# Kernel optimization log

Measured on AMD Instinct MI355X. Metric: run time of the kernel, lower is better.

## Reference

```python
import jax, jax.numpy as jnp
import numpy as np

BN_EPS = 1e-5
L1_EPS = 1e-12


def setup_inputs() -> dict:
    key = jax.random.key(0)
    k1, k2, k3, k4 = jax.random.split(key, 4)
    B, N, M, F = 16, 2048, 12, 64
    bond = 128
    atom = jax.random.normal(k1, (B, N, F), dtype=jnp.float32)
    adj = jax.random.randint(k2, (B, N * M, 2), 0, N, dtype=jnp.int64)
    stdv = 1.0 / np.sqrt(bond)
    W = jax.random.uniform(k3, (2 * F, bond), dtype=jnp.float32, minval=-stdv, maxval=stdv)
    b = jax.random.uniform(k4, (bond,), dtype=jnp.float32, minval=-stdv, maxval=stdv)
    gamma = jnp.ones((bond,), dtype=jnp.float32)
    beta = jnp.zeros((bond,), dtype=jnp.float32)
    return {"atom": atom, "adj": adj, "W": W, "b": b, "gamma": gamma, "beta": beta}


def reference(atom, adj, W, b, gamma, beta):
    B, N, F = atom.shape
    # flatten the (E,2) index pairs and gather atom features: (B, 2E, F)
    idx = adj.reshape(B, -1)
    gathered = jnp.take_along_axis(atom, idx[:, :, None], axis=1)
    # pair features per edge: (B, E, 2F)
    x = gathered.reshape(B, -1, 2 * F)
    # L1 normalize along the edge dim (dim=-2), matching F.normalize(p=1, dim=-2)
    denom = jnp.maximum(jnp.sum(jnp.abs(x), axis=1, keepdims=True), L1_EPS)
    x = x / denom
    # linear: (B, E, bond)
    x = jnp.einsum('bef,fc->bec', x, W) + b
    # BatchNorm1d (training mode): stats over batch and edge dims per channel
    mean = jnp.mean(x, axis=(0, 1))
    var = jnp.mean(jnp.square(x - mean), axis=(0, 1))  # biased variance
    x = (x - mean) * jax.lax.rsqrt(var + BN_EPS) * gamma + beta
    return jnp.tanh(x)
```

## Files before the change

kernel.cpp:

```cpp
#include <hip/hip_runtime.h>

#define B 16
#define N 2048
#define F 64
#define E 24576
#define C 128

typedef unsigned int uint32;
typedef unsigned short ushort16;
typedef float fvec4 __attribute__((ext_vector_type(4)));
typedef int   ivec2 __attribute__((ext_vector_type(2)));


__device__ __forceinline__ ushort16 f2bf(float f) {
    uint32 u = __float_as_uint(f);
    u += 0x7fffu + ((u >> 16) & 1u);
    return (ushort16)(u >> 16);
}
__device__ __forceinline__ float bf_lo(uint32 v) { return __uint_as_float(v << 16); }
__device__ __forceinline__ float bf_hi(uint32 v) { return __uint_as_float(v & 0xffff0000u); }

__global__ __launch_bounds__(256) void k_count(const int* __restrict__ adj,
                                               int* __restrict__ cnt) {
    int i = blockIdx.x * 256 + threadIdx.x;
    int n = adj[i];
    int k = i & 1;
    int b = i / (E * 2);
    atomicAdd(&cnt[(b * N + n) * 2 + k], 1);
}

__global__ __launch_bounds__(256) void k_denom(const float* __restrict__ atom,
                                               const int* __restrict__ cnt,
                                               float* __restrict__ denom) {
    int bid = blockIdx.x;
    int b = bid & 15;
    int chunk = bid >> 4;
    int t = threadIdx.x;
    int ch = t & 127;
    int sub = t >> 7;
    int half = ch >> 6;
    int f = ch & 63;
    float s = 0.f;
    int n0 = chunk * 128 + sub * 64;
    for (int j = 0; j < 64; ++j) {
        int n = n0 + j;
        float cf = (float)cnt[(b * N + n) * 2 + half];
        s = fmaf(cf, fabsf(atom[(b * N + n) * 64 + f]), s);
    }
    __shared__ float sd[256];
    sd[t] = s;
    __syncthreads();
    if (t < 128) atomicAdd(&denom[b * C + ch], sd[t] + sd[t + 128]);
}

__global__ __launch_bounds__(256, 2) void k_p(const float* __restrict__ atom,
                                              const float* __restrict__ W,
                                              const float* __restrict__ denom,
                                              const int* __restrict__ cnt,
                                              ushort16* __restrict__ P,
                                              float* __restrict__ nodew,
                                              float* __restrict__ nodesq) {
    int bid = blockIdx.x;
    int b = bid & 15;
    int chunk = bid >> 4;
    int t = threadIdx.x;
    int cp = t & 127;
    int half = cp >> 6;
    int c = cp & 63;
    int sub = t >> 7;

    __shared__ float invd[128];
    __shared__ float A2[64 * 128];
    __shared__ float cnts[2][64];

    if (t < 128) invd[t] = 1.0f / fmaxf(denom[b * C + t], 1e-12f);
    int nbase = chunk * 64;
    if (t < 128) {
        int h = t >> 6, r = t & 63;
        cnts[h][r] = (float)cnt[(b * N + nbase + r) * 2 + h];
    }
    __syncthreads();

    for (int i = t; i < 64 * 128; i += 256) {
        int r = i >> 7, col = i & 127;
        float a = atom[(b * N + nbase + r) * 64 + (col & 63)];
        A2[i] = a * invd[col];
    }

    float wreg0[64], wreg1[64];
#pragma unroll
    for (int f = 0; f < 64; ++f) {
        wreg0[f] = W[(half * 64 + f) * 128 + c];
        wreg1[f] = W[(half * 64 + f) * 128 + c + 64];
    }

    __syncthreads();

    float s1a = 0.f, s2a = 0.f, s1b = 0.f, s2b = 0.f;
    int r0 = sub * 32;
    for (int r = r0; r < r0 + 32; ++r) {
        const float* a = &A2[r * 128 + half * 64];
        float acc0 = 0.f, acc1 = 0.f;
#pragma unroll
        for (int f = 0; f < 64; f += 4) {
            float4 av = *(const float4*)(a + f);
            acc0 = fmaf(av.x, wreg0[f], acc0);
            acc0 = fmaf(av.y, wreg0[f + 1], acc0);
            acc0 = fmaf(av.z, wreg0[f + 2], acc0);
            acc0 = fmaf(av.w, wreg0[f + 3], acc0);
            acc1 = fmaf(av.x, wreg1[f], acc1);
            acc1 = fmaf(av.y, wreg1[f + 1], acc1);
            acc1 = fmaf(av.z, wreg1[f + 2], acc1);
            acc1 = fmaf(av.w, wreg1[f + 3], acc1);
        }
        float cw = cnts[half][r];
        s1a = fmaf(cw, acc0, s1a);
        s2a = fmaf(cw * acc0, acc0, s2a);
        s1b = fmaf(cw, acc1, s1b);
        s2b = fmaf(cw * acc1, acc1, s2b);
        size_t base = ((size_t)(b * N + nbase + r)) * 256 + half * 128;
        P[base + c]      = f2bf(acc0);
        P[base + c + 64] = f2bf(acc1);
    }
    atomicAdd(&nodew[b * 256 + half * 128 + c],      s1a);
    atomicAdd(&nodew[b * 256 + half * 128 + c + 64], s1b);
    atomicAdd(&nodesq[b * 128 + c],      s2a);
    atomicAdd(&nodesq[b * 128 + c + 64], s2b);
}

__global__ __launch_bounds__(256) void k_out(const ivec2* __restrict__ adj2,
                                             const uint2* __restrict__ Pu2,
                                             const float* __restrict__ nodew,
                                             const float* __restrict__ nodesq,
                                             const float* __restrict__ gamma,
                                             const float* __restrict__ beta,
                                             fvec4* __restrict__ out4) {
    int bid = blockIdx.x;
    int b = bid & 15;
    int chunk = bid >> 4;
    int t = threadIdx.x;
    __shared__ float ssc[128], ssh[128];
    __shared__ ivec2 eadj[512];

    int e0 = chunk * 512;
    const ivec2* ab = &adj2[(size_t)b * E + e0];
    eadj[t]       = __builtin_nontemporal_load(&ab[t]);
    eadj[t + 256] = __builtin_nontemporal_load(&ab[t + 256]);

    if (t < 128) {
        int cch = t;
        float m = 0.f, q = 0.f;
        const float invE = 1.0f / (float)E;
#pragma unroll
        for (int b2 = 0; b2 < B; ++b2) {
            float S0 = nodew[b2 * 256 + cch];
            float S1 = nodew[b2 * 256 + 128 + cch];
            m += S0 + S1;
            q += nodesq[b2 * 128 + cch] + 2.0f * S0 * S1 * invE;
        }
        const float inv = 1.0f / (float)(B * E);
        float mean_d = m * inv;
        float var = fmaxf(q * inv - mean_d * mean_d, 0.f);
        float sc = gamma[cch] * rsqrtf(var + 1e-5f);
        ssc[cch] = sc;
        ssh[cch] = beta[cch] - mean_d * sc;
    }
    __syncthreads();

    int g = t >> 6;
    int l = t & 63;
    int esub = l >> 5;
    int c4 = l & 31;
    float sc0 = ssc[4 * c4],     sh0 = ssh[4 * c4];
    float sc1 = ssc[4 * c4 + 1], sh1 = ssh[4 * c4 + 1];
    float sc2 = ssc[4 * c4 + 2], sh2 = ssh[4 * c4 + 2];
    float sc3 = ssc[4 * c4 + 3], sh3 = ssh[4 * c4 + 3];
#pragma unroll 4
    for (int i = 0; i < 64; ++i) {
        int ei = i * 8 + g * 2 + esub;
        ivec2 nn = eadj[ei];
        uint2 v0 = Pu2[((size_t)(b * N + nn.x)) * 64 + c4];
        uint2 v1 = Pu2[((size_t)(b * N + nn.y)) * 64 + 32 + c4];
        float d0 = bf_lo(v0.x) + bf_lo(v1.x);
        float d1 = bf_hi(v0.x) + bf_hi(v1.x);
        float d2 = bf_lo(v0.y) + bf_lo(v1.y);
        float d3 = bf_hi(v0.y) + bf_hi(v1.y);
        float x0 = fmaf(d0, sc0, sh0);
        float x1 = fmaf(d1, sc1, sh1);
        float x2 = fmaf(d2, sc2, sh2);
        float x3 = fmaf(d3, sc3, sh3);
        fvec4 o;
        o.x = 1.0f - 2.0f * __builtin_amdgcn_rcpf(__expf(2.0f * x0) + 1.0f);
        o.y = 1.0f - 2.0f * __builtin_amdgcn_rcpf(__expf(2.0f * x1) + 1.0f);
        o.z = 1.0f - 2.0f * __builtin_amdgcn_rcpf(__expf(2.0f * x2) + 1.0f);
        o.w = 1.0f - 2.0f * __builtin_amdgcn_rcpf(__expf(2.0f * x3) + 1.0f);
        __builtin_nontemporal_store(o, &out4[((size_t)(b * E + e0 + ei)) * 32 + c4]);
    }
}

extern "C" void kernel_launch(void* const* d_in, const int* in_sizes, int n_in,
                              void* d_out, int out_size, void* d_ws, size_t ws_size,
                              hipStream_t stream) {
    const float* atom  = (const float*)d_in[0];
    const int*   adj   = (const int*)d_in[1];
    const float* W     = (const float*)d_in[2];
    const float* gamma = (const float*)d_in[4];
    const float* beta  = (const float*)d_in[5];
    float* out = (float*)d_out;
    float* ws  = (float*)d_ws;

    int*      cnt    = (int*)ws;
    float*    denom  = ws + 65536;
    float*    nodew  = ws + 67584;
    float*    nodesq = ws + 71680;
    ushort16* P      = (ushort16*)(ws + 73984);

    (void)hipMemsetAsync(d_ws, 0, 294912, stream);
    k_count<<<3072, 256, 0, stream>>>(adj, cnt);
    k_denom<<<256,  256, 0, stream>>>(atom, cnt, denom);
    k_p    <<<512,  256, 0, stream>>>(atom, W, denom, cnt, P, nodew, nodesq);
    k_out  <<<768,  256, 0, stream>>>((const ivec2*)adj, (const uint2*)P,
                                      nodew, nodesq, gamma, beta, (fvec4*)out);
}
```

Measured before the change: 287.2 us.

## Histogram adjacency counts in LDS, split BN stats kernel, widen output gather

k_count now builds a per-batch node histogram in shared memory and flushes only the nonzero bins to global memory. This replaces about 786k global atomics with far fewer. The BatchNorm scale and shift are computed once in a tiny separate kernel, prescaled for exp2, instead of being recomputed by every k_out block. k_out now has each thread load 16-byte P vectors and produce 8 channels per edge, using exp2 for tanh. This halves the gather instruction count, at the cost of an extra kernel launch and more register use.

```diff
diff --git a/kernel.cpp b/kernel.cpp
--- a/kernel.cpp
+++ b/kernel.cpp
@@ -22,11 +22,22 @@
 
 __global__ __launch_bounds__(256) void k_count(const int* __restrict__ adj,
                                                int* __restrict__ cnt) {
-    int i = blockIdx.x * 256 + threadIdx.x;
-    int n = adj[i];
-    int k = i & 1;
-    int b = i / (E * 2);
-    atomicAdd(&cnt[(b * N + n) * 2 + k], 1);
+    __shared__ int h[N * 2];
+    int t = threadIdx.x;
+    for (int i = t; i < N * 2; i += 256) h[i] = 0;
+    __syncthreads();
+    int b = blockIdx.x & 15;
+    int part = blockIdx.x >> 4;
+    const int* ab = adj + (size_t)b * E * 2 + part * 12288;
+    for (int i = t; i < 12288; i += 256) {
+        int n = ab[i];
+        atomicAdd(&h[n * 2 + (i & 1)], 1);
+    }
+    __syncthreads();
+    for (int i = t; i < N * 2; i += 256) {
+        int v = h[i];
+        if (v) atomicAdd(&cnt[b * N * 2 + i], v);
+    }
 }
 
 __global__ __launch_bounds__(256) void k_denom(const float* __restrict__ atom,
@@ -128,18 +139,39 @@
     atomicAdd(&nodesq[b * 128 + c + 64], s2b);
 }
 
+__global__ __launch_bounds__(128) void k_stats(const float* __restrict__ nodew,
+                                               const float* __restrict__ nodesq,
+                                               const float* __restrict__ gamma,
+                                               const float* __restrict__ beta,
+                                               float* __restrict__ st) {
+    int cch = threadIdx.x;
+    float m = 0.f, q = 0.f;
+    const float invE = 1.0f / (float)E;
+#pragma unroll
+    for (int b2 = 0; b2 < B; ++b2) {
+        float S0 = nodew[b2 * 256 + cch];
+        float S1 = nodew[b2 * 256 + 128 + cch];
+        m += S0 + S1;
+        q += nodesq[b2 * 128 + cch] + 2.0f * S0 * S1 * invE;
+    }
+    const float inv = 1.0f / (float)(B * E);
+    float mean_d = m * inv;
+    float var = fmaxf(q * inv - mean_d * mean_d, 0.f);
+    float sc = gamma[cch] * rsqrtf(var + 1e-5f);
+    float sh = beta[cch] - mean_d * sc;
+    const float C2 = 2.8853900817779268f;
+    st[cch]       = sc * C2;
+    st[128 + cch] = sh * C2;
+}
+
 __global__ __launch_bounds__(256) void k_out(const ivec2* __restrict__ adj2,
-                                             const uint2* __restrict__ Pu2,
-                                             const float* __restrict__ nodew,
-                                             const float* __restrict__ nodesq,
-                                             const float* __restrict__ gamma,
-                                             const float* __restrict__ beta,
+                                             const uint4* __restrict__ Pu4,
+                                             const float* __restrict__ st,
                                              fvec4* __restrict__ out4) {
     int bid = blockIdx.x;
     int b = bid & 15;
     int chunk = bid >> 4;
     int t = threadIdx.x;
-    __shared__ float ssc[128], ssh[128];
     __shared__ ivec2 eadj[512];
 
     int e0 = chunk * 512;
@@ -147,54 +179,48 @@
     eadj[t]       = __builtin_nontemporal_load(&ab[t]);
     eadj[t + 256] = __builtin_nontemporal_load(&ab[t + 256]);
 
-    if (t < 128) {
-        int cch = t;
-        float m = 0.f, q = 0.f;
-        const float invE = 1.0f / (float)E;
-#pragma unroll
-        for (int b2 = 0; b2 < B; ++b2) {
-            float S0 = nodew[b2 * 256 + cch];
-            float S1 = nodew[b2 * 256 + 128 + cch];
-            m += S0 + S1;
-            q += nodesq[b2 * 128 + cch] + 2.0f * S0 * S1 * invE;
-        }
-        const float inv = 1.0f / (float)(B * E);
-        float mean_d = m * inv;
-        float var = fmaxf(q * inv - mean_d * mean_d, 0.f);
-        float sc = gamma[cch] * rsqrtf(var + 1e-5f);
-        ssc[cch] = sc;
-        ssh[cch] = beta[cch] - mean_d * sc;
-    }
-    __syncthreads();
-
-    int g = t >> 6;
-    int l = t & 63;
-    int esub = l >> 5;
-    int c4 = l & 31;
-    float sc0 = ssc[4 * c4],     sh0 = ssh[4 * c4];
-    float sc1 = ssc[4 * c4 + 1], sh1 = ssh[4 * c4 + 1];
-    float sc2 = ssc[4 * c4 + 2], sh2 = ssh[4 * c4 + 2];
-    float sc3 = ssc[4 * c4 + 3], sh3 = ssh[4 * c4 + 3];
-#pragma unroll 4
-    for (int i = 0; i < 64; ++i) {
-        int ei = i * 8 + g * 2 + esub;
+    int c8 = t & 15;
+    int eg = t >> 4;
+    float4 sca = *(const float4*)(st + c8 * 8);
+    float4 scb = *(const float4*)(st + c8 * 8 + 4);
+    float4 sha = *(const float4*)(st + 128 + c8 * 8);
+    float4 shb = *(const float4*)(st + 128 + c8 * 8 + 4);
+    __syncthreads();
+
+#pragma unroll 2
+    for (int i = 0; i < 32; ++i) {
+        int ei = i * 16 + eg;
         ivec2 nn = eadj[ei];
-        uint2 v0 = Pu2[((size_t)(b * N + nn.x)) * 64 + c4];
-        uint2 v1 = Pu2[((size_t)(b * N + nn.y)) * 64 + 32 + c4];
+        uint4 v0 = Pu4[((size_t)(b * N + nn.x)) * 32 + c8];
+        uint4 v1 = Pu4[((size_t)(b * N + nn.y)) * 32 + 16 + c8];
         float d0 = bf_lo(v0.x) + bf_lo(v1.x);
         float d1 = bf_hi(v0.x) + bf_hi(v1.x);
         float d2 = bf_lo(v0.y) + bf_lo(v1.y);
         float d3 = bf_hi(v0.y) + bf_hi(v1.y);
-        float x0 = fmaf(d0, sc0, sh0);
-        float x1 = fmaf(d1, sc1, sh1);
-        float x2 = fmaf(d2, sc2, sh2);
-        float x3 = fmaf(d3, sc3, sh3);
-        fvec4 o;
-        o.x = 1.0f - 2.0f * __builtin_amdgcn_rcpf(__expf(2.0f * x0) + 1.0f);
-        o.y = 1.0f - 2.0f * __builtin_amdgcn_rcpf(__expf(2.0f * x1) + 1.0f);
-        o.z = 1.0f - 2.0f * __builtin_amdgcn_rcpf(__expf(2.0f * x2) + 1.0f);
-        o.w = 1.0f - 2.0f * __builtin_amdgcn_rcpf(__expf(2.0f * x3) + 1.0f);
-        __builtin_nontemporal_store(o, &out4[((size_t)(b * E + e0 + ei)) * 32 + c4]);
+        float d4 = bf_lo(v0.z) + bf_lo(v1.z);
+        float d5 = bf_hi(v0.z) + bf_hi(v1.z);
+        float d6 = bf_lo(v0.w) + bf_lo(v1.w);
+        float d7 = bf_hi(v0.w) + bf_hi(v1.w);
+        float x0 = fmaf(d0, sca.x, sha.x);
+        float x1 = fmaf(d1, sca.y, sha.y);
+        float x2 = fmaf(d2, sca.z, sha.z);
+        float x3 = fmaf(d3, sca.w, sha.w);
+        float x4 = fmaf(d4, scb.x, shb.x);
+        float x5 = fmaf(d5, scb.y, shb.y);
+        float x6 = fmaf(d6, scb.z, shb.z);
+        float x7 = fmaf(d7, scb.w, shb.w);
+        fvec4 oa, ob;
+        oa.x = fmaf(-2.0f, __builtin_amdgcn_rcpf(__builtin_amdgcn_exp2f(x0) + 1.0f), 1.0f);
+        oa.y = fmaf(-2.0f, __builtin_amdgcn_rcpf(__builtin_amdgcn_exp2f(x1) + 1.0f), 1.0f);
+        oa.z = fmaf(-2.0f, __builtin_amdgcn_rcpf(__builtin_amdgcn_exp2f(x2) + 1.0f), 1.0f);
+        oa.w = fmaf(-2.0f, __builtin_amdgcn_rcpf(__builtin_amdgcn_exp2f(x3) + 1.0f), 1.0f);
+        ob.x = fmaf(-2.0f, __builtin_amdgcn_rcpf(__builtin_amdgcn_exp2f(x4) + 1.0f), 1.0f);
+        ob.y = fmaf(-2.0f, __builtin_amdgcn_rcpf(__builtin_amdgcn_exp2f(x5) + 1.0f), 1.0f);
+        ob.z = fmaf(-2.0f, __builtin_amdgcn_rcpf(__builtin_amdgcn_exp2f(x6) + 1.0f), 1.0f);
+        ob.w = fmaf(-2.0f, __builtin_amdgcn_rcpf(__builtin_amdgcn_exp2f(x7) + 1.0f), 1.0f);
+        size_t obase = ((size_t)(b * E + e0 + ei)) * 32 + c8 * 2;
+        __builtin_nontemporal_store(oa, &out4[obase]);
+        __builtin_nontemporal_store(ob, &out4[obase + 1]);
     }
 }
 
@@ -213,12 +239,13 @@
     float*    denom  = ws + 65536;
     float*    nodew  = ws + 67584;
     float*    nodesq = ws + 71680;
+    float*    st     = ws + 73728;
     ushort16* P      = (ushort16*)(ws + 73984);
 
     (void)hipMemsetAsync(d_ws, 0, 294912, stream);
-    k_count<<<3072, 256, 0, stream>>>(adj, cnt);
+    k_count<<<64,   256, 0, stream>>>(adj, cnt);
     k_denom<<<256,  256, 0, stream>>>(atom, cnt, denom);
     k_p    <<<512,  256, 0, stream>>>(atom, W, denom, cnt, P, nodew, nodesq);
-    k_out  <<<768,  256, 0, stream>>>((const ivec2*)adj, (const uint2*)P,
-                                      nodew, nodesq, gamma, beta, (fvec4*)out);
-}
+    k_stats<<<1,    128, 0, stream>>>(nodew, nodesq, gamma, beta, st);
+    k_out  <<<768,  256, 0, stream>>>((const ivec2*)adj, (const uint4*)P, st, (fvec4*)out);
+}
```

Measured after the change: 328.3 us. +14.3%, slower.
